# Kernel tuning notes

Measured on AMD Instinct MI355X. Metric: run time of the kernel, lower is better.

## Reference

```python
import jax, jax.numpy as jnp
import numpy as np
import math

N_HEADS = 16
ROPE_THETA = 10000.0
NEG_INF = -1e30


def setup_inputs() -> dict:
    key = jax.random.key(0)
    k1, k2, k3, k4 = jax.random.split(key, 4)
    B, S, D = 2, 2048, 2048
    x = jax.random.normal(k1, (B, S, D), dtype=jnp.float32)
    qkv = 0.01 * jax.random.normal(k2, (2 * D, D), dtype=jnp.float32)
    H = N_HEADS
    dh = D // H
    nope = dh // 2
    rope = dh // 2
    wk = 0.01 * jax.random.normal(k3, (H * nope + rope, D), dtype=jnp.float32)
    wo = 0.01 * jax.random.normal(k4, (D, D), dtype=jnp.float32)
    return {"x": x, "qkv": qkv, "wk": wk, "wo": wo}


def _rope_cos_sin(S, dh, rope_dim, dtype):
    # freqs over full dh as in the torch module, then sliced to rope_dim//2 and tiled x2
    freqs = 1.0 / (ROPE_THETA ** (jnp.arange(0, dh, 2).astype(jnp.float32) / dh))
    emb = jnp.arange(S, dtype=jnp.float32)[:, None] * freqs[None, :]  # [S, dh//2]
    cos = jnp.tile(jnp.cos(emb)[:, : rope_dim // 2], (1, 2))[None, None]  # [1,1,S,rope]
    sin = jnp.tile(jnp.sin(emb)[:, : rope_dim // 2], (1, 2))[None, None]
    return cos.astype(dtype), sin.astype(dtype)


def _apply_rope(xq, cos, sin):
    x1, x2 = jnp.split(xq, 2, axis=-1)
    return xq * cos + jnp.concatenate([-x2, x1], axis=-1) * sin


def reference(x, qkv, wk, wo):
    B, S, D = x.shape
    H = N_HEADS
    dh = D // H
    nope = dh // 2
    rope = dh // 2

    QV = x @ qkv.T                              # [B,S,2D]
    Q, V = jnp.split(QV, 2, axis=-1)
    Q = Q.reshape(B, S, H, dh).transpose(0, 2, 1, 3)        # [B,H,S,dh]
    v_heads = V.reshape(B, S, H, dh).transpose(0, 2, 1, 3)  # [B,H,S,dh]
    Qn, Qr = Q[..., :nope], Q[..., nope:]

    K = x @ wk.T                                # [B,S,H*nope+rope]
    Kn = K[..., : H * nope].reshape(B, S, H, nope).transpose(0, 2, 1, 3)  # [B,H,S,nope]
    Kr = K[..., H * nope :].reshape(B, S, 1, rope).transpose(0, 2, 1, 3)  # [B,1,S,rope]

    cos, sin = _rope_cos_sin(S, dh, rope, x.dtype)
    Qr = _apply_rope(Qr, cos, sin)
    Kr = _apply_rope(Kr, cos, sin)

    q_heads = jnp.concatenate([Qn, Qr], axis=-1)                               # [B,H,S,dh]
    k_heads = jnp.concatenate([Kn, jnp.broadcast_to(Kr, (B, H, S, rope))], -1)  # [B,H,S,dh]

    scale = 1.0 / math.sqrt(dh)
    scores = jnp.einsum('bhqd,bhkd->bhqk', q_heads, k_heads) * scale
    mask = jnp.tril(jnp.ones((S, S), dtype=bool))
    scores = jnp.where(mask[None, None], scores, NEG_INF)
    attn = jax.nn.softmax(scores, axis=-1)
    out = jnp.einsum('bhqk,bhkd->bhqd', attn, v_heads)
    out = out.transpose(0, 2, 1, 3).reshape(B, S, D) @ wo.T
    return (out, k_heads, v_heads)
```

## Files before the change

kernel.cpp:

```cpp
#include <hip/hip_runtime.h>
#include <hip/hip_bf16.h>


typedef unsigned short u16;
typedef unsigned int u32;
typedef __bf16 bf16x8 __attribute__((ext_vector_type(8)));
typedef float f32x4 __attribute__((ext_vector_type(4)));

__device__ __forceinline__ u16 f2bf(float x) {
  union { __hip_bfloat16 h; u16 u; } c;
  c.h = __float2bfloat16(x);
  return c.u;
}
__device__ __forceinline__ float bf2f(u16 u) {
  union { u32 u; float f; } c;
  c.u = ((u32)u) << 16;
  return c.f;
}
__device__ __forceinline__ f32x4 mfma16(bf16x8 a, bf16x8 b, f32x4 c) {
  return __builtin_amdgcn_mfma_f32_16x16x32_bf16(a, b, c, 0, 0, 0);
}
__device__ __forceinline__ void gload_lds16(const void* g, void* l) {
  __builtin_amdgcn_global_load_lds((__attribute__((address_space(1))) void*)g,
                                   (__attribute__((address_space(3))) void*)l,
                                   16, 0, 0);
}

__global__ __launch_bounds__(256) void cast_all(const float4* __restrict__ x,
                                                const float4* __restrict__ qkv,
                                                const float* __restrict__ wk,
                                                const float4* __restrict__ wo,
                                                u16* __restrict__ x_bf,
                                                u16* __restrict__ wcomb,
                                                u16* __restrict__ wo_bf) {
  int i = blockIdx.x * blockDim.x + threadIdx.x;
  const float4* src;
  u16* dst;
  int j;
  if (i < 2097152) {
    src = x; dst = x_bf; j = i;
  } else if (i < 4194304) {
    src = qkv; dst = wcomb; j = i - 2097152;
  } else if (i < 4849664) {
    j = i - 4194304;
    int r = (j * 4) >> 11;
    u32 lo = 0, hi = 0;
    if (r < 1088) {
      float4 v = ((const float4*)wk)[j];
      lo = (u32)f2bf(v.x) | ((u32)f2bf(v.y) << 16);
      hi = (u32)f2bf(v.z) | ((u32)f2bf(v.w) << 16);
    }
    ((uint2*)(wcomb + 8388608))[j] = make_uint2(lo, hi);
    return;
  } else {
    src = wo; dst = wo_bf; j = i - 4849664;
  }
  float4 v = src[j];
  u32 lo = (u32)f2bf(v.x) | ((u32)f2bf(v.y) << 16);
  u32 hi = (u32)f2bf(v.z) | ((u32)f2bf(v.w) << 16);
  ((uint2*)dst)[j] = make_uint2(lo, hi);
}

__device__ __forceinline__ void cstore(u16* C, size_t i, float v) { C[i] = f2bf(v); }
__device__ __forceinline__ void cstore(float* C, size_t i, float v) { C[i] = v; }

template <typename CT, int BM>
__global__ __launch_bounds__(512, 2) void gemm256(const u16* __restrict__ A,
                                                  const u16* __restrict__ W,
                                                  CT* __restrict__ C,
                                                  int M, int N, int K) {
  constexpr int MI = BM / 64;
  constexpr int AH = BM * 64;
  constexpr int AL = BM / 128;
  constexpr int BOFF = 4 * AH;
  __shared__ char lds[BOFF + 65536];
  const int tid = threadIdx.x;
  const int wid = tid >> 6, lane = tid & 63;
  const int lr = lane & 15, lg = lane >> 4;
  const int wr = wid >> 2, wc = wid & 3;
  const int xorv = (lr & 7) << 4;
  const int nwg = gridDim.x * gridDim.y;
  const int lin = blockIdx.y * gridDim.x + blockIdx.x;
  const int swz = (lin & 7) * (nwg >> 3) + (lin >> 3);
  const int m0 = (swz / gridDim.x) * BM;
  const int n0 = (swz % gridDim.x) * 256;
  const int nkt = K >> 6;

  f32x4 acc[2 * MI][4] = {};
  bf16x8 a[MI][2], b[4][2];

  const int o0 = tid * 16, o1 = 8192 + tid * 16;
  const int r0 = o0 >> 7, c0 = ((o0 & 127) ^ ((r0 & 7) << 4)) >> 1;
  const int r1 = o1 >> 7, c1 = ((o1 & 127) ^ ((r1 & 7) << 4)) >> 1;
  const u16* gA0[2] = {A + (size_t)(m0 + r0) * K + c0,
                       A + (size_t)(m0 + BM / 2 + r0) * K + c0};
  const u16* gA1[2] = {A + (size_t)(m0 + r1) * K + c1,
                       A + (size_t)(m0 + BM / 2 + r1) * K + c1};
  const u16* gB0[2] = {W + (size_t)(n0 + r0) * K + c0,
                       W + (size_t)(n0 + 128 + r0) * K + c0};
  const u16* gB1[2] = {W + (size_t)(n0 + r1) * K + c1,
                       W + (size_t)(n0 + 128 + r1) * K + c1};

  auto STAGEA = [&](int t, int h) {
    char* d_ = lds + (t & 1) * (2 * AH) + h * AH + wid * 1024;
    gload_lds16(gA0[h] + (size_t)t * 64, d_);
    if constexpr (AL == 2) gload_lds16(gA1[h] + (size_t)t * 64, d_ + 8192);
  };
  auto STAGEB = [&](int t, int h) {
    char* d_ = lds + BOFF + (t & 1) * 32768 + h * 16384 + wid * 1024;
    gload_lds16(gB0[h] + (size_t)t * 64, d_);
    gload_lds16(gB1[h] + (size_t)t * 64, d_ + 8192);
  };
  auto WAITKEEP = [&]() {
    if constexpr (BM == 256) asm volatile("s_waitcnt vmcnt(4)" ::: "memory");
    else asm volatile("s_waitcnt vmcnt(3)" ::: "memory");
  };

  STAGEA(0, 0); STAGEB(0, 0); STAGEA(0, 1); STAGEB(0, 1);
  if (nkt > 1) { STAGEA(1, 0); STAGEB(1, 0); }
  WAITKEEP();
  __builtin_amdgcn_s_barrier();

  for (int t = 0; t < nkt; ++t) {
    const char* Ab = lds + (t & 1) * (2 * AH);
    const char* Bb = lds + BOFF + (t & 1) * 32768;
    const int arow = wr * (BM / 4), brow = wc * 32;
#pragma unroll
    for (int mi = 0; mi < MI; mi++)
#pragma unroll
      for (int ks = 0; ks < 2; ks++)
        a[mi][ks] = *(const bf16x8*)(Ab + (arow + mi * 16 + lr) * 128 + ((lg * 16 + ks * 64) ^ xorv));
#pragma unroll
    for (int ni = 0; ni < 2; ni++)
#pragma unroll
      for (int ks = 0; ks < 2; ks++)
        b[ni][ks] = *(const bf16x8*)(Bb + (brow + ni * 16 + lr) * 128 + ((lg * 16 + ks * 64) ^ xorv));
    if (t + 1 < nkt) STAGEA(t + 1, 1);
    __builtin_amdgcn_s_barrier();
    asm volatile("s_waitcnt lgkmcnt(0)" ::: "memory");
    __builtin_amdgcn_sched_barrier(0);
    __builtin_amdgcn_s_setprio(1);
#pragma unroll
    for (int mi = 0; mi < MI; mi++)
#pragma unroll
      for (int ni = 0; ni < 2; ni++)
#pragma unroll
        for (int ks = 0; ks < 2; ks++)
          acc[mi][ni] = mfma16(a[mi][ks], b[ni][ks], acc[mi][ni]);
    __builtin_amdgcn_s_setprio(0);
    __builtin_amdgcn_s_barrier();
#pragma unroll
    for (int ni = 0; ni < 2; ni++)
#pragma unroll
      for (int ks = 0; ks < 2; ks++)
        b[2 + ni][ks] = *(const bf16x8*)(Bb + 16384 + (brow + ni * 16 + lr) * 128 + ((lg * 16 + ks * 64) ^ xorv));
    if (t + 1 < nkt) STAGEB(t + 1, 1);
    __builtin_amdgcn_s_barrier();
    asm volatile("s_waitcnt lgkmcnt(0)" ::: "memory");
    __builtin_amdgcn_sched_barrier(0);
    __builtin_amdgcn_s_setprio(1);
#pragma unroll
    for (int mi = 0; mi < MI; mi++)
#pragma unroll
      for (int ni = 0; ni < 2; ni++)
#pragma unroll
        for (int ks = 0; ks < 2; ks++)
          acc[mi][2 + ni] = mfma16(a[mi][ks], b[2 + ni][ks], acc[mi][2 + ni]);
    __builtin_amdgcn_s_setprio(0);
    __builtin_amdgcn_s_barrier();
#pragma unroll
    for (int mi = 0; mi < MI; mi++)
#pragma unroll
      for (int ks = 0; ks < 2; ks++)
        a[mi][ks] = *(const bf16x8*)(Ab + AH + (arow + mi * 16 + lr) * 128 + ((lg * 16 + ks * 64) ^ xorv));
    if (t + 2 < nkt) STAGEA(t + 2, 0);
    __builtin_amdgcn_s_barrier();
    asm volatile("s_waitcnt lgkmcnt(0)" ::: "memory");
    __builtin_amdgcn_sched_barrier(0);
    __builtin_amdgcn_s_setprio(1);
#pragma unroll
    for (int mi = 0; mi < MI; mi++)
#pragma unroll
      for (int ni = 0; ni < 2; ni++)
#pragma unroll
        for (int ks = 0; ks < 2; ks++)
          acc[MI + mi][ni] = mfma16(a[mi][ks], b[ni][ks], acc[MI + mi][ni]);
    __builtin_amdgcn_s_setprio(0);
    __builtin_amdgcn_s_barrier();
    if (t + 2 < nkt) {
      STAGEB(t + 2, 0);
      WAITKEEP();
    } else if (t + 1 < nkt) {
      asm volatile("s_waitcnt vmcnt(0)" ::: "memory");
    }
    __builtin_amdgcn_s_barrier();
    asm volatile("s_waitcnt lgkmcnt(0)" ::: "memory");
    __builtin_amdgcn_sched_barrier(0);
    __builtin_amdgcn_s_setprio(1);
#pragma unroll
    for (int mi = 0; mi < MI; mi++)
#pragma unroll
      for (int ni = 0; ni < 2; ni++)
#pragma unroll
        for (int ks = 0; ks < 2; ks++)
          acc[MI + mi][2 + ni] = mfma16(a[mi][ks], b[2 + ni][ks], acc[MI + mi][2 + ni]);
    __builtin_amdgcn_s_setprio(0);
    __builtin_amdgcn_s_barrier();
  }

#pragma unroll
  for (int Mh = 0; Mh < 2; Mh++)
#pragma unroll
    for (int mi = 0; mi < MI; mi++) {
      int row = m0 + Mh * (BM / 2) + wr * (BM / 4) + mi * 16 + lg * 4;
#pragma unroll
      for (int Nh = 0; Nh < 2; Nh++)
#pragma unroll
        for (int ni = 0; ni < 2; ni++) {
          int col = n0 + Nh * 128 + wc * 32 + ni * 16 + lr;
#pragma unroll
          for (int r = 0; r < 4; r++)
            cstore(C, (size_t)(row + r) * N + col, acc[Mh * MI + mi][Nh * 2 + ni][r]);
        }
    }
}

__global__ __launch_bounds__(256) void rope_scatter2(u16* __restrict__ QVK,
                                                     u16* __restrict__ kh,
                                                     float* __restrict__ k_out, int S) {
  const int row = blockIdx.x;
  const int b = row >> 11, s = row & 2047;
  const int tid = threadIdx.x;
  __shared__ float kr[64];
  const float LOG1E4_64 = 0.14391156511f;
  u16* qrow = QVK + (size_t)row * 5376;
  if (tid < 32) {
    float freq = __expf(-(float)tid * LOG1E4_64);
    float sn, c;
    __sincosf((float)s * freq, &sn, &c);
    float a = bf2f(qrow[5120 + tid]);
    float bb = bf2f(qrow[5152 + tid]);
    kr[tid] = a * c - bb * sn;
    kr[tid + 32] = bb * c + a * sn;
  }
  for (int idx = tid; idx < 512; idx += 256) {
    int h = idx >> 5, jj = idx & 31;
    float freq = __expf(-(float)jj * LOG1E4_64);
    float sn, c;
    __sincosf((float)s * freq, &sn, &c);
    u16* p1 = qrow + h * 128 + 64 + jj;
    u16* p2 = qrow + h * 128 + 96 + jj;
    float x1 = bf2f(*p1), x2 = bf2f(*p2);
    *p1 = f2bf(x1 * c - x2 * sn);
    *p2 = f2bf(x2 * c + x1 * sn);
  }
  __syncthreads();
  for (int idx = tid; idx < 2048; idx += 256) {
    int h = idx >> 7, d = idx & 127;
    float val = (d < 64) ? bf2f(qrow[4096 + h * 64 + d]) : kr[d - 64];
    size_t o = ((size_t)(b * 16 + h) * S + s) * 128 + d;
    kh[o] = f2bf(val);
    k_out[o] = val;
  }
}

__global__ __launch_bounds__(256) void v_scatter(const u16* __restrict__ QVK,
                                                 u16* __restrict__ vt,
                                                 float* __restrict__ v_out, int S) {
  const int blk = blockIdx.x;
  const int st = blk & 63;
  const int dt = (blk >> 6) & 3;
  const int bh = blk >> 8;
  const int b = bh >> 4, h = bh & 15;
  __shared__ u16 t[32][34];
  const int tx = threadIdx.x & 31, ty = threadIdx.x >> 5;
  const int s0 = st * 32, d0 = dt * 32;
#pragma unroll
  for (int i = 0; i < 4; i++) {
    int sl = ty + 8 * i;
    u16 u = QVK[(size_t)(b * S + s0 + sl) * 5376 + 2048 + h * 128 + d0 + tx];
    t[sl][tx] = u;
    v_out[((size_t)bh * S + s0 + sl) * 128 + d0 + tx] = bf2f(u);
  }
  __syncthreads();
#pragma unroll
  for (int i = 0; i < 4; i++) {
    int dl = ty + 8 * i;
    vt[((size_t)bh * 128 + d0 + dl) * S + s0 + tx] = t[tx][dl];
  }
}

__global__ __launch_bounds__(512) void flash_attn3(const u16* __restrict__ QVK,
                                                   const u16* __restrict__ Kh,
                                                   const u16* __restrict__ Vt,
                                                   u16* __restrict__ attn, int S) {
  __shared__ char lds[49152];
  const int tid = threadIdx.x, wid = tid >> 6, lane = tid & 63;
  const int bh = blockIdx.x & 31;
  const int qb = 15 - (int)(blockIdx.x >> 5);
  const int q0 = qb * 128 + wid * 16;
  const int b = bh >> 4, h = bh & 15;
  const int q = lane & 15, g = lane >> 4;
  const u16* Qb = QVK + (size_t)b * S * 5376 + h * 128;
  const u16* Kb = Kh + (size_t)bh * S * 128;
  const u16* Vb = Vt + (size_t)bh * 128 * S;
  const int qg = q0 + q;
  const int xr = (q & 7) << 4;

  const u16* srcK[2];
  const u16* srcV[2];
#pragma unroll
  for (int i = 0; i < 2; i++) {
    int o = ((i * 8 + wid) << 10) | (lane << 4);
    int rK = o >> 8, cbK = (o & 255) ^ ((rK & 7) << 4);
    srcK[i] = Kb + rK * 128 + (cbK >> 1);
    int dV = o >> 7, kbV = (o & 127) ^ ((dV & 7) << 4);
    srcV[i] = Vb + (size_t)dV * S + (kbV >> 1);
  }

  bf16x8 qf[4];
#pragma unroll
  for (int f = 0; f < 4; f++)
    qf[f] = *(const bf16x8*)(Qb + (size_t)qg * 5376 + f * 32 + g * 8);

  f32x4 acc[8] = {};
  float m = -INFINITY, l = 0.f;
  const float sc = 0.08838834764831845f;
  const int ktiles = 2 * qb + 2;

#pragma unroll
  for (int i = 0; i < 2; i++) {
    char* ld = lds + ((i * 8 + wid) << 10);
    gload_lds16(srcK[i], ld);
    gload_lds16(srcV[i], ld + 32768);
  }
  asm volatile("s_waitcnt vmcnt(0)" ::: "memory");
  __builtin_amdgcn_s_barrier();

  for (int kt = 0; kt < ktiles; ++kt) {
    const char* Kt = lds + (kt & 1) * 16384;
    const char* Vl = lds + 32768;
    const bool more = (kt + 1 < ktiles);
    if (more) {
#pragma unroll
      for (int i = 0; i < 2; i++)
        gload_lds16(srcK[i] + (size_t)(kt + 1) * 8192,
                    lds + (((kt & 1) ^ 1) << 14) + ((i * 8 + wid) << 10));
      asm volatile("s_waitcnt vmcnt(4)" ::: "memory");
    } else {
      asm volatile("s_waitcnt vmcnt(2)" ::: "memory");
    }
    __builtin_amdgcn_s_barrier();

    f32x4 s[4] = {};
    const char* Kq = Kt + q * 256;
    __builtin_amdgcn_s_setprio(1);
#pragma unroll
    for (int f = 0; f < 4; f++) {
#pragma unroll
      for (int c = 0; c < 4; c++) {
        bf16x8 kf = *(const bf16x8*)(Kq + c * 4096 + ((f * 64 + g * 16) ^ xr));
        s[c] = mfma16(kf, qf[f], s[c]);
      }
    }
    __builtin_amdgcn_s_setprio(0);

    const int kbg = kt * 64;
    float v[16];
    const bool maskt = (kbg + 63 > q0);
#pragma unroll
    for (int c = 0; c < 4; c++)
#pragma unroll
      for (int r = 0; r < 4; r++) {
        float x = s[c][r];
        if (maskt && (kbg + c * 16 + g * 4 + r > qg)) x = -1e30f;
        v[c * 4 + r] = x;
      }
    float tm = v[0];
#pragma unroll
    for (int i = 1; i < 16; i++) tm = fmaxf(tm, v[i]);
    tm = fmaxf(tm, __shfl_xor(tm, 16));
    tm = fmaxf(tm, __shfl_xor(tm, 32));
    if (!__all(tm <= m + 64.0f)) {
      float mnew = fmaxf(m, tm);
      float corr = __expf((m - mnew) * sc);
      m = mnew;
      l *= corr;
      float corr_r[4];
#pragma unroll
      for (int r = 0; r < 4; r++)
        corr_r[r] = __shfl(corr, (lane & 48) | (g * 4 + r));
#pragma unroll
      for (int j = 0; j < 8; j++)
#pragma unroll
        for (int r = 0; r < 4; r++) acc[j][r] *= corr_r[r];
    }
    const float nms = -m * sc;
    float p[16], ts = 0.f;
#pragma unroll
    for (int i = 0; i < 16; i++) {
      p[i] = __expf(fmaf(v[i], sc, nms));
      ts += p[i];
    }
    ts += __shfl_xor(ts, 16);
    ts += __shfl_xor(ts, 32);
    l += ts;

    const int src0 = q | ((g & 1) << 5);
    const bool hi = (g & 2);
    union { u32 u[4]; bf16x8 v; } pcA, pcB;
    {
      u32 w0a = (u32)f2bf(p[0]) | ((u32)f2bf(p[1]) << 16);
      u32 w0b = (u32)f2bf(p[2]) | ((u32)f2bf(p[3]) << 16);
      u32 w1a = (u32)f2bf(p[4]) | ((u32)f2bf(p[5]) << 16);
      u32 w1b = (u32)f2bf(p[6]) | ((u32)f2bf(p[7]) << 16);
      u32 a_lo  = (u32)__shfl((int)w0a, src0);
      u32 b_lo  = (u32)__shfl((int)w0b, src0);
      u32 a_lo2 = (u32)__shfl((int)w0a, src0 + 16);
      u32 b_lo2 = (u32)__shfl((int)w0b, src0 + 16);
      u32 a_hi  = (u32)__shfl((int)w1a, src0);
      u32 b_hi  = (u32)__shfl((int)w1b, src0);
      u32 a_hi2 = (u32)__shfl((int)w1a, src0 + 16);
      u32 b_hi2 = (u32)__shfl((int)w1b, src0 + 16);
      pcA.u[0] = hi ? a_hi : a_lo;
      pcA.u[1] = hi ? b_hi : b_lo;
      pcA.u[2] = hi ? a_hi2 : a_lo2;
      pcA.u[3] = hi ? b_hi2 : b_lo2;
    }
    {
      u32 w0a = (u32)f2bf(p[8])  | ((u32)f2bf(p[9])  << 16);
      u32 w0b = (u32)f2bf(p[10]) | ((u32)f2bf(p[11]) << 16);
      u32 w1a = (u32)f2bf(p[12]) | ((u32)f2bf(p[13]) << 16);
      u32 w1b = (u32)f2bf(p[14]) | ((u32)f2bf(p[15]) << 16);
      u32 a_lo  = (u32)__shfl((int)w0a, src0);
      u32 b_lo  = (u32)__shfl((int)w0b, src0);
      u32 a_lo2 = (u32)__shfl((int)w0a, src0 + 16);
      u32 b_lo2 = (u32)__shfl((int)w0b, src0 + 16);
      u32 a_hi  = (u32)__shfl((int)w1a, src0);
      u32 b_hi  = (u32)__shfl((int)w1b, src0);
      u32 a_hi2 = (u32)__shfl((int)w1a, src0 + 16);
      u32 b_hi2 = (u32)__shfl((int)w1b, src0 + 16);
      pcB.u[0] = hi ? a_hi : a_lo;
      pcB.u[1] = hi ? b_hi : b_lo;
      pcB.u[2] = hi ? a_hi2 : a_lo2;
      pcB.u[3] = hi ? b_hi2 : b_lo2;
    }

    if (more) asm volatile("s_waitcnt vmcnt(2)" ::: "memory");
    else      asm volatile("s_waitcnt vmcnt(0)" ::: "memory");
    __builtin_amdgcn_s_barrier();

    const int vcolA = (g * 16) ^ xr;
    const int vcolB = (64 + g * 16) ^ xr;
    __builtin_amdgcn_s_setprio(1);
#pragma unroll
    for (int j = 0; j < 8; j++) {
      bf16x8 vfA = *(const bf16x8*)(Vl + (j * 16 + q) * 128 + vcolA);
      acc[j] = mfma16(pcA.v, vfA, acc[j]);
    }
#pragma unroll
    for (int j = 0; j < 8; j++) {
      bf16x8 vfB = *(const bf16x8*)(Vl + (j * 16 + q) * 128 + vcolB);
      acc[j] = mfma16(pcB.v, vfB, acc[j]);
    }
    __builtin_amdgcn_s_setprio(0);

    __builtin_amdgcn_s_barrier();
    if (more) {
#pragma unroll
      for (int i = 0; i < 2; i++)
        gload_lds16(srcV[i] + (size_t)(kt + 1) * 64,
                    lds + 32768 + ((i * 8 + wid) << 10));
    }
  }

  float linv = 1.0f / l;
  float linv_r[4];
#pragma unroll
  for (int r = 0; r < 4; r++)
    linv_r[r] = __shfl(linv, (lane & 48) | (g * 4 + r));
  u16* ab = attn + (size_t)(b * S + q0) * 2048 + h * 128;
#pragma unroll
  for (int j = 0; j < 8; j++)
#pragma unroll
    for (int r = 0; r < 4; r++)
      ab[(size_t)(g * 4 + r) * 2048 + j * 16 + q] = f2bf(acc[j][r] * linv_r[r]);
}

extern "C" void kernel_launch(void* const* d_in, const int* in_sizes, int n_in,
                              void* d_out, int out_size, void* d_ws, size_t ws_size,
                              hipStream_t stream) {
  (void)in_sizes; (void)n_in; (void)out_size; (void)ws_size;
  const int S = 2048;
  const float* x = (const float*)d_in[0];
  const float* qkv = (const float*)d_in[1];
  const float* wk = (const float*)d_in[2];
  const float* wo = (const float*)d_in[3];
  float* out = (float*)d_out;
  float* k_out = out + (size_t)8388608;
  float* v_out = out + (size_t)16777216;

  char* ws = (char*)d_ws;
  u16* x_bf  = (u16*)(ws + 0);
  u16* wcomb = (u16*)(ws + 16777216);
  u16* wo_bf = (u16*)(ws + 38797312);
  u16* qvk   = (u16*)(ws + 47185920);
  u16* vt_bf = (u16*)(ws + 91226112);
  u16* attn_bf = x_bf;
  u16* k_bf = wcomb;

  cast_all<<<23040, 256, 0, stream>>>((const float4*)x, (const float4*)qkv, wk,
                                      (const float4*)wo, x_bf, wcomb, wo_bf);

  gemm256<u16, 128><<<dim3(21, 32), 512, 0, stream>>>(x_bf, wcomb, qvk, 4096, 5376, 2048);
  rope_scatter2<<<4096, 256, 0, stream>>>(qvk, k_bf, k_out, S);
  v_scatter<<<8192, 256, 0, stream>>>(qvk, vt_bf, v_out, S);
  flash_attn3<<<512, 512, 0, stream>>>(qvk, k_bf, vt_bf, attn_bf, S);
  gemm256<float, 128><<<dim3(8, 32), 512, 0, stream>>>(attn_bf, wo_bf, out, 4096, 2048, 2048);
}
```

Baseline: 287.2 us.

## Split QKV GEMM into 256x256 and 256x128 tiles, route P through LDS

After: 279.6 us. 1.03x faster.

```diff
diff --git a/kernel.cpp b/kernel.cpp
--- a/kernel.cpp
+++ b/kernel.cpp
@@ -16,6 +16,9 @@
   union { u32 u; float f; } c;
   c.u = ((u32)u) << 16;
   return c.f;
+}
+__device__ __forceinline__ u32 pack2(float a, float b) {
+  return (u32)f2bf(a) | ((u32)f2bf(b) << 16);
 }
 __device__ __forceinline__ f32x4 mfma16(bf16x8 a, bf16x8 b, f32x4 c) {
   return __builtin_amdgcn_mfma_f32_16x16x32_bf16(a, b, c, 0, 0, 0);
@@ -47,8 +50,8 @@
     u32 lo = 0, hi = 0;
     if (r < 1088) {
       float4 v = ((const float4*)wk)[j];
-      lo = (u32)f2bf(v.x) | ((u32)f2bf(v.y) << 16);
-      hi = (u32)f2bf(v.z) | ((u32)f2bf(v.w) << 16);
+      lo = pack2(v.x, v.y);
+      hi = pack2(v.z, v.w);
     }
     ((uint2*)(wcomb + 8388608))[j] = make_uint2(lo, hi);
     return;
@@ -56,24 +59,25 @@
     src = wo; dst = wo_bf; j = i - 4849664;
   }
   float4 v = src[j];
-  u32 lo = (u32)f2bf(v.x) | ((u32)f2bf(v.y) << 16);
-  u32 hi = (u32)f2bf(v.z) | ((u32)f2bf(v.w) << 16);
-  ((uint2*)dst)[j] = make_uint2(lo, hi);
+  ((uint2*)dst)[j] = make_uint2(pack2(v.x, v.y), pack2(v.z, v.w));
 }
 
 __device__ __forceinline__ void cstore(u16* C, size_t i, float v) { C[i] = f2bf(v); }
 __device__ __forceinline__ void cstore(float* C, size_t i, float v) { C[i] = v; }
 
-template <typename CT, int BM>
+template <typename CT, int BM, int BN>
 __global__ __launch_bounds__(512, 2) void gemm256(const u16* __restrict__ A,
                                                   const u16* __restrict__ W,
                                                   CT* __restrict__ C,
                                                   int M, int N, int K) {
   constexpr int MI = BM / 64;
+  constexpr int NI = BN / 128;
   constexpr int AH = BM * 64;
+  constexpr int BH = BN * 64;
   constexpr int AL = BM / 128;
+  constexpr int BL = BN / 128;
   constexpr int BOFF = 4 * AH;
-  __shared__ char lds[BOFF + 65536];
+  __shared__ char lds[BOFF + 4 * BH];
   const int tid = threadIdx.x;
   const int wid = tid >> 6, lane = tid & 63;
   const int lr = lane & 15, lg = lane >> 4;
@@ -83,11 +87,11 @@
   const int lin = blockIdx.y * gridDim.x + blockIdx.x;
   const int swz = (lin & 7) * (nwg >> 3) + (lin >> 3);
   const int m0 = (swz / gridDim.x) * BM;
-  const int n0 = (swz % gridDim.x) * 256;
+  const int n0 = (swz % gridDim.x) * BN;
   const int nkt = K >> 6;
 
-  f32x4 acc[2 * MI][4] = {};
-  bf16x8 a[MI][2], b[4][2];
+  f32x4 acc[2 * MI][2 * NI] = {};
+  bf16x8 a[MI][2], b[2 * NI][2];
 
   const int o0 = tid * 16, o1 = 8192 + tid * 16;
   const int r0 = o0 >> 7, c0 = ((o0 & 127) ^ ((r0 & 7) << 4)) >> 1;
@@ -97,9 +101,9 @@
   const u16* gA1[2] = {A + (size_t)(m0 + r1) * K + c1,
                        A + (size_t)(m0 + BM / 2 + r1) * K + c1};
   const u16* gB0[2] = {W + (size_t)(n0 + r0) * K + c0,
-                       W + (size_t)(n0 + 128 + r0) * K + c0};
+                       W + (size_t)(n0 + BN / 2 + r0) * K + c0};
   const u16* gB1[2] = {W + (size_t)(n0 + r1) * K + c1,
-                       W + (size_t)(n0 + 128 + r1) * K + c1};
+                       W + (size_t)(n0 + BN / 2 + r1) * K + c1};
 
   auto STAGEA = [&](int t, int h) {
     char* d_ = lds + (t & 1) * (2 * AH) + h * AH + wid * 1024;
@@ -107,12 +111,12 @@
     if constexpr (AL == 2) gload_lds16(gA1[h] + (size_t)t * 64, d_ + 8192);
   };
   auto STAGEB = [&](int t, int h) {
-    char* d_ = lds + BOFF + (t & 1) * 32768 + h * 16384 + wid * 1024;
+    char* d_ = lds + BOFF + (t & 1) * (2 * BH) + h * BH + wid * 1024;
     gload_lds16(gB0[h] + (size_t)t * 64, d_);
-    gload_lds16(gB1[h] + (size_t)t * 64, d_ + 8192);
+    if constexpr (BL == 2) gload_lds16(gB1[h] + (size_t)t * 64, d_ + 8192);
   };
   auto WAITKEEP = [&]() {
-    if constexpr (BM == 256) asm volatile("s_waitcnt vmcnt(4)" ::: "memory");
+    if constexpr (AL + BL == 4) asm volatile("s_waitcnt vmcnt(4)" ::: "memory");
     else asm volatile("s_waitcnt vmcnt(3)" ::: "memory");
   };
 
@@ -123,15 +127,15 @@
 
   for (int t = 0; t < nkt; ++t) {
     const char* Ab = lds + (t & 1) * (2 * AH);
-    const char* Bb = lds + BOFF + (t & 1) * 32768;
-    const int arow = wr * (BM / 4), brow = wc * 32;
+    const char* Bb = lds + BOFF + (t & 1) * (2 * BH);
+    const int arow = wr * (BM / 4), brow = wc * (BN / 8);
 #pragma unroll
     for (int mi = 0; mi < MI; mi++)
 #pragma unroll
       for (int ks = 0; ks < 2; ks++)
         a[mi][ks] = *(const bf16x8*)(Ab + (arow + mi * 16 + lr) * 128 + ((lg * 16 + ks * 64) ^ xorv));
 #pragma unroll
-    for (int ni = 0; ni < 2; ni++)
+    for (int ni = 0; ni < NI; ni++)
 #pragma unroll
       for (int ks = 0; ks < 2; ks++)
         b[ni][ks] = *(const bf16x8*)(Bb + (brow + ni * 16 + lr) * 128 + ((lg * 16 + ks * 64) ^ xorv));
@@ -143,17 +147,17 @@
 #pragma unroll
     for (int mi = 0; mi < MI; mi++)
 #pragma unroll
-      for (int ni = 0; ni < 2; ni++)
+      for (int ni = 0; ni < NI; ni++)
 #pragma unroll
         for (int ks = 0; ks < 2; ks++)
           acc[mi][ni] = mfma16(a[mi][ks], b[ni][ks], acc[mi][ni]);
     __builtin_amdgcn_s_setprio(0);
     __builtin_amdgcn_s_barrier();
 #pragma unroll
-    for (int ni = 0; ni < 2; ni++)
+    for (int ni = 0; ni < NI; ni++)
 #pragma unroll
       for (int ks = 0; ks < 2; ks++)
-        b[2 + ni][ks] = *(const bf16x8*)(Bb + 16384 + (brow + ni * 16 + lr) * 128 + ((lg * 16 + ks * 64) ^ xorv));
+        b[NI + ni][ks] = *(const bf16x8*)(Bb + BH + (brow + ni * 16 + lr) * 128 + ((lg * 16 + ks * 64) ^ xorv));
     if (t + 1 < nkt) STAGEB(t + 1, 1);
     __builtin_amdgcn_s_barrier();
     asm volatile("s_waitcnt lgkmcnt(0)" ::: "memory");
@@ -162,10 +166,10 @@
 #pragma unroll
     for (int mi = 0; mi < MI; mi++)
 #pragma unroll
-      for (int ni = 0; ni < 2; ni++)
+      for (int ni = 0; ni < NI; ni++)
 #pragma unroll
         for (int ks = 0; ks < 2; ks++)
-          acc[mi][2 + ni] = mfma16(a[mi][ks], b[2 + ni][ks], acc[mi][2 + ni]);
+          acc[mi][NI + ni] = mfma16(a[mi][ks], b[NI + ni][ks], acc[mi][NI + ni]);
     __builtin_amdgcn_s_setprio(0);
     __builtin_amdgcn_s_barrier();
 #pragma unroll
@@ -181,7 +185,7 @@
 #pragma unroll
     for (int mi = 0; mi < MI; mi++)
 #pragma unroll
-      for (int ni = 0; ni < 2; ni++)
+      for (int ni = 0; ni < NI; ni++)
 #pragma unroll
         for (int ks = 0; ks < 2; ks++)
           acc[MI + mi][ni] = mfma16(a[mi][ks], b[ni][ks], acc[MI + mi][ni]);
@@ -200,10 +204,10 @@
 #pragma unroll
     for (int mi = 0; mi < MI; mi++)
 #pragma unroll
-      for (int ni = 0; ni < 2; ni++)
+      for (int ni = 0; ni < NI; ni++)
 #pragma unroll
         for (int ks = 0; ks < 2; ks++)
-          acc[MI + mi][2 + ni] = mfma16(a[mi][ks], b[2 + ni][ks], acc[MI + mi][2 + ni]);
+          acc[MI + mi][NI + ni] = mfma16(a[mi][ks], b[NI + ni][ks], acc[MI + mi][NI + ni]);
     __builtin_amdgcn_s_setprio(0);
     __builtin_amdgcn_s_barrier();
   }
@@ -216,11 +220,11 @@
 #pragma unroll
       for (int Nh = 0; Nh < 2; Nh++)
 #pragma unroll
-        for (int ni = 0; ni < 2; ni++) {
-          int col = n0 + Nh * 128 + wc * 32 + ni * 16 + lr;
+        for (int ni = 0; ni < NI; ni++) {
+          int col = n0 + Nh * (BN / 2) + wc * (BN / 8) + ni * 16 + lr;
 #pragma unroll
           for (int r = 0; r < 4; r++)
-            cstore(C, (size_t)(row + r) * N + col, acc[Mh * MI + mi][Nh * 2 + ni][r]);
+            cstore(C, (size_t)(row + r) * N + col, acc[Mh * MI + mi][Nh * NI + ni][r]);
         }
     }
 }
@@ -290,11 +294,11 @@
   }
 }
 
-__global__ __launch_bounds__(512) void flash_attn3(const u16* __restrict__ QVK,
+__global__ __launch_bounds__(512) void flash_attn4(const u16* __restrict__ QVK,
                                                    const u16* __restrict__ Kh,
                                                    const u16* __restrict__ Vt,
                                                    u16* __restrict__ attn, int S) {
-  __shared__ char lds[49152];
+  __shared__ char lds[49152 + 8 * 2304];
   const int tid = threadIdx.x, wid = tid >> 6, lane = tid & 63;
   const int bh = blockIdx.x & 31;
   const int qb = 15 - (int)(blockIdx.x >> 5);
@@ -306,6 +310,7 @@
   const u16* Vb = Vt + (size_t)bh * 128 * S;
   const int qg = q0 + q;
   const int xr = (q & 7) << 4;
+  char* const Pw = lds + 49152 + wid * 2304 + q * 144;
 
   const u16* srcK[2];
   const u16* srcV[2];
@@ -406,45 +411,16 @@
     ts += __shfl_xor(ts, 32);
     l += ts;
 
-    const int src0 = q | ((g & 1) << 5);
-    const bool hi = (g & 2);
-    union { u32 u[4]; bf16x8 v; } pcA, pcB;
-    {
-      u32 w0a = (u32)f2bf(p[0]) | ((u32)f2bf(p[1]) << 16);
-      u32 w0b = (u32)f2bf(p[2]) | ((u32)f2bf(p[3]) << 16);
-      u32 w1a = (u32)f2bf(p[4]) | ((u32)f2bf(p[5]) << 16);
-      u32 w1b = (u32)f2bf(p[6]) | ((u32)f2bf(p[7]) << 16);
-      u32 a_lo  = (u32)__shfl((int)w0a, src0);
-      u32 b_lo  = (u32)__shfl((int)w0b, src0);
-      u32 a_lo2 = (u32)__shfl((int)w0a, src0 + 16);
-      u32 b_lo2 = (u32)__shfl((int)w0b, src0 + 16);
-      u32 a_hi  = (u32)__shfl((int)w1a, src0);
-      u32 b_hi  = (u32)__shfl((int)w1b, src0);
-      u32 a_hi2 = (u32)__shfl((int)w1a, src0 + 16);
-      u32 b_hi2 = (u32)__shfl((int)w1b, src0 + 16);
-      pcA.u[0] = hi ? a_hi : a_lo;
-      pcA.u[1] = hi ? b_hi : b_lo;
-      pcA.u[2] = hi ? a_hi2 : a_lo2;
-      pcA.u[3] = hi ? b_hi2 : b_lo2;
-    }
-    {
-      u32 w0a = (u32)f2bf(p[8])  | ((u32)f2bf(p[9])  << 16);
-      u32 w0b = (u32)f2bf(p[10]) | ((u32)f2bf(p[11]) << 16);
-      u32 w1a = (u32)f2bf(p[12]) | ((u32)f2bf(p[13]) << 16);
-      u32 w1b = (u32)f2bf(p[14]) | ((u32)f2bf(p[15]) << 16);
-      u32 a_lo  = (u32)__shfl((int)w0a, src0);
-      u32 b_lo  = (u32)__shfl((int)w0b, src0);
-      u32 a_lo2 = (u32)__shfl((int)w0a, src0 + 16);
-      u32 b_lo2 = (u32)__shfl((int)w0b, src0 + 16);
-      u32 a_hi  = (u32)__shfl((int)w1a, src0);
-      u32 b_hi  = (u32)__shfl((int)w1b, src0);
-      u32 a_hi2 = (u32)__shfl((int)w1a, src0 + 16);
-      u32 b_hi2 = (u32)__shfl((int)w1b, src0 + 16);
-      pcB.u[0] = hi ? a_hi : a_lo;
-      pcB.u[1] = hi ? b_hi : b_lo;
-      pcB.u[2] = hi ? a_hi2 : a_lo2;
-      pcB.u[3] = hi ? b_hi2 : b_lo2;
-    }
+#pragma unroll
+    for (int c = 0; c < 4; c++) {
+      int off = (c * 32 + g * 8) ^ xr;
+      *(uint2*)(Pw + off) = make_uint2(pack2(p[c * 4], p[c * 4 + 1]),
+                                       pack2(p[c * 4 + 2], p[c * 4 + 3]));
+    }
+    asm volatile("s_waitcnt lgkmcnt(0)" ::: "memory");
+    __builtin_amdgcn_sched_barrier(0);
+    bf16x8 pcA = *(const bf16x8*)(Pw + ((g * 16) ^ xr));
+    bf16x8 pcB = *(const bf16x8*)(Pw + ((64 + g * 16) ^ xr));
 
     if (more) asm volatile("s_waitcnt vmcnt(2)" ::: "memory");
     else      asm volatile("s_waitcnt vmcnt(0)" ::: "memory");
@@ -456,12 +432,12 @@
 #pragma unroll
     for (int j = 0; j < 8; j++) {
       bf16x8 vfA = *(const bf16x8*)(Vl + (j * 16 + q) * 128 + vcolA);
-      acc[j] = mfma16(pcA.v, vfA, acc[j]);
+      acc[j] = mfma16(pcA, vfA, acc[j]);
     }
 #pragma unroll
     for (int j = 0; j < 8; j++) {
       bf16x8 vfB = *(const bf16x8*)(Vl + (j * 16 + q) * 128 + vcolB);
-      acc[j] = mfma16(pcB.v, vfB, acc[j]);
+      acc[j] = mfma16(pcB, vfB, acc[j]);
     }
     __builtin_amdgcn_s_setprio(0);
 
@@ -512,9 +488,13 @@
   cast_all<<<23040, 256, 0, stream>>>((const float4*)x, (const float4*)qkv, wk,
                                       (const float4*)wo, x_bf, wcomb, wo_bf);
 
-  gemm256<u16, 128><<<dim3(21, 32), 512, 0, stream>>>(x_bf, wcomb, qvk, 4096, 5376, 2048);
+  gemm256<u16, 256, 256><<<dim3(16, 16), 512, 0, stream>>>(x_bf, wcomb, qvk,
+                                                           4096, 5376, 2048);
+  gemm256<u16, 256, 128><<<dim3(10, 16), 512, 0, stream>>>(
+      x_bf, wcomb + (size_t)4096 * 2048, qvk + 4096, 4096, 5376, 2048);
   rope_scatter2<<<4096, 256, 0, stream>>>(qvk, k_bf, k_out, S);
   v_scatter<<<8192, 256, 0, stream>>>(qvk, vt_bf, v_out, S);
-  flash_attn3<<<512, 512, 0, stream>>>(qvk, k_bf, vt_bf, attn_bf, S);
-  gemm256<float, 128><<<dim3(8, 32), 512, 0, stream>>>(attn_bf, wo_bf, out, 4096, 2048, 2048);
-}
+  flash_attn4<<<512, 512, 0, stream>>>(qvk, k_bf, vt_bf, attn_bf, S);
+  gemm256<float, 128, 256><<<dim3(8, 32), 512, 0, stream>>>(attn_bf, wo_bf, out,
+                                                            4096, 2048, 2048);
+}
```
